# Kernel tuning notes

Hardware: AMD Instinct MI355X
Metric: run time of the kernel (lower is better)

## Reference

```python
import jax, jax.numpy as jnp
import numpy as np

B, D, L, H = 256, 512, 64, 300


def setup_inputs() -> dict:
    key = jax.random.key(0)
    ks = jax.random.split(key, 16)
    s = 0.05  # weight init scale to keep activations sane through ReLU chains
    return {
        "x": jax.random.normal(ks[0], (B, D), jnp.float32),
        "eps": jax.random.normal(ks[1], (B, L), jnp.float32),
        "W": jax.random.normal(ks[2], (D, L), jnp.float32) * s,
        "enc1_w": jax.random.normal(ks[3], (H, D), jnp.float32) * s,
        "enc1_b": jax.random.normal(ks[4], (H,), jnp.float32) * s,
        "enc2_w": jax.random.normal(ks[5], (H, H), jnp.float32) * s,
        "enc2_b": jax.random.normal(ks[6], (H,), jnp.float32) * s,
        "zm_w": jax.random.normal(ks[7], (L, H), jnp.float32) * s,
        "zm_b": jax.random.normal(ks[8], (L,), jnp.float32) * s,
        "zv_w": jax.random.normal(ks[9], (L, H), jnp.float32) * s,
        "zv_b": jax.random.normal(ks[10], (L,), jnp.float32) * s,
        "gen1_w": jax.random.normal(ks[11], (H, L), jnp.float32) * s,
        "gen2_w": jax.random.normal(ks[12], (H, H), jnp.float32) * s,
        "gen2_b": jax.random.normal(ks[13], (H,), jnp.float32) * s,
        "head_w": jax.random.normal(ks[14], (D, H), jnp.float32) * s,
        "head_b": jax.random.normal(ks[15], (D,), jnp.float32) * s,
    }


def reference(x, eps, W, enc1_w, enc1_b, enc2_w, enc2_b, zm_w, zm_b,
              zv_w, zv_b, gen1_w, gen2_w, gen2_b, head_w, head_b):
    # encode: q_z = ReLU(Linear) -> ReLU(Linear)
    h = jax.nn.relu(x @ enc1_w.T + enc1_b)
    h = jax.nn.relu(h @ enc2_w.T + enc2_b)
    z_mean = h @ zm_w.T + zm_b          # [B, L]
    z_log_var = h @ zv_w.T + zv_b       # [B, L]
    # reparameterize (eps passed in for determinism)
    z = z_mean + eps * jnp.exp(0.5 * z_log_var)
    # decode: per-column masked z through shared generator + per-column head,
    # vectorized over the column axis D (mask = W rows)
    masked = z[:, None, :] * W[None, :, :]                       # [B, D, L]
    g1 = jax.nn.relu(jnp.einsum('bdl,hl->bdh', masked, gen1_w))  # [B, D, H]
    g2 = jax.nn.relu(jnp.einsum('bdh,gh->bdg', g1, gen2_w) + gen2_b)
    x_mean = jnp.einsum('bdh,dh->bd', g2, head_w) + head_b       # [B, D]
    return (x_mean, z, z_mean, z_log_var)
```

## Files before the change

kernel.cpp:

```cpp
#include <hip/hip_runtime.h>

typedef unsigned short u16;
typedef unsigned int u32;

typedef __bf16 bf16x8 __attribute__((ext_vector_type(8)));
typedef float f32x4 __attribute__((ext_vector_type(4)));

union V16 { uint4 u; bf16x8 v; u16 s[8]; __bf16 h[8]; };
union F4  { float4 v; float f[4]; };

__device__ __forceinline__ float bf2f(u16 a) {
  union { u32 u; float f; } c; c.u = ((u32)a) << 16; return c.f;
}

#define Z_OFF   131072
#define ZM_OFF  147456
#define ZLV_OFF 163840

#define B1_OFF 0
#define B2_OFF 2560
#define E1_OFF 15360
#define E2_OFF 35840
#define ZMP_OFF 48640
#define ZVP_OFF 51200
#define FRAG_TOTAL 53760
#define WB4  53760
#define XB4  57856
#define H1_4 74240
#define H2_4 84480
#define PACK_THREADS (FRAG_TOTAL + 4096 + 16384)

__device__ __forceinline__ void pack_one(const float* __restrict__ src,
                                         int t, int s, int lane,
                                         int Nsrc, int Ksrc, int rowlen,
                                         uint4* __restrict__ dst) {
  const int n = t * 16 + (lane & 15);
  const int k0 = s * 32 + ((lane >> 4) << 3);
  V16 v;
#pragma unroll
  for (int j = 0; j < 8; ++j) {
    const int k = k0 + j;
    v.h[j] = (n < Nsrc && k < Ksrc) ? (__bf16)src[n * rowlen + k] : (__bf16)0.f;
  }
  *dst = v.u;
}

__device__ __forceinline__ void cvt8(const float* __restrict__ src, uint4* __restrict__ dst) {
  F4 a, b; a.v = *(const float4*)src; b.v = *(const float4*)(src + 4);
  V16 v;
#pragma unroll
  for (int j = 0; j < 4; ++j) { v.h[j] = (__bf16)a.f[j]; v.h[4 + j] = (__bf16)b.f[j]; }
  *dst = v.u;
}

__global__ __launch_bounds__(256) void pack_kernel(
    const float* __restrict__ g1w, const float* __restrict__ g2w,
    const float* __restrict__ e1w, const float* __restrict__ e2w,
    const float* __restrict__ zmw, const float* __restrict__ zvw,
    const float* __restrict__ W,   const float* __restrict__ x,
    uint4* __restrict__ ws4) {
  const int idx = blockIdx.x * 256 + threadIdx.x;
  if (idx >= PACK_THREADS) return;
  const int lane = idx & 63;
  if (idx < B2_OFF) {
    const int f = (idx - B1_OFF) >> 6;
    pack_one(g1w, f >> 1, f & 1, lane, 300, 64, 64, ws4 + idx);
  } else if (idx < E1_OFF) {
    const int f = (idx - B2_OFF) >> 6;
    pack_one(g2w, f / 10, f % 10, lane, 300, 300, 300, ws4 + idx);
  } else if (idx < E2_OFF) {
    const int f = (idx - E1_OFF) >> 6;
    pack_one(e1w, f >> 4, f & 15, lane, 300, 512, 512, ws4 + idx);
  } else if (idx < ZMP_OFF) {
    const int f = (idx - E2_OFF) >> 6;
    pack_one(e2w, f / 10, f % 10, lane, 300, 300, 300, ws4 + idx);
  } else if (idx < ZVP_OFF) {
    const int f = (idx - ZMP_OFF) >> 6;
    pack_one(zmw, f / 10, f % 10, lane, 64, 300, 300, ws4 + idx);
  } else if (idx < FRAG_TOTAL) {
    const int f = (idx - ZVP_OFF) >> 6;
    pack_one(zvw, f / 10, f % 10, lane, 64, 300, 300, ws4 + idx);
  } else if (idx < FRAG_TOTAL + 4096) {
    const int i = idx - FRAG_TOTAL;
    cvt8(W + i * 8, ws4 + WB4 + i);
  } else {
    const int i = idx - FRAG_TOTAL - 4096;
    cvt8(x + i * 8, ws4 + XB4 + i);
  }
}

__global__ __launch_bounds__(256) void enc1_kernel(
    const uint4* __restrict__ xb, const uint4* __restrict__ e1p,
    const float* __restrict__ e1b, u16* __restrict__ h1) {
  __shared__ float red[4 * 320];
  const int wg = blockIdx.x;
  const int rt = wg / 20, nt = wg % 20;
  const int tid = threadIdx.x;
  const int w = tid >> 6, lane = tid & 63, q = lane >> 4, c = lane & 15;
  f32x4 acc = {0.f, 0.f, 0.f, 0.f};
  const int arow = rt * 16 + c;
#pragma unroll
  for (int j = 0; j < 4; ++j) {
    const int s = 4 * w + j;
    V16 a, b;
    a.u = xb[arow * 64 + s * 4 + q];
    b.u = e1p[(nt * 16 + s) * 64 + lane];
    acc = __builtin_amdgcn_mfma_f32_16x16x32_bf16(a.v, b.v, acc, 0, 0, 0);
  }
#pragma unroll
  for (int i = 0; i < 4; ++i) red[w * 320 + lane * 5 + i] = acc[i];
  __syncthreads();
  const int col = nt * 16 + c;
  float t = 0.f;
#pragma unroll
  for (int ww = 0; ww < 4; ++ww) t += red[ww * 320 + lane * 5 + w];
  const float bias = (col < 300) ? e1b[col] : 0.f;
  const int row = rt * 16 + 4 * q + w;
  V16 o; o.h[0] = (col < 300) ? (__bf16)fmaxf(t + bias, 0.f) : (__bf16)0.f;
  h1[row * 320 + col] = o.s[0];
}

__global__ __launch_bounds__(320) void enc2_kernel(
    const uint4* __restrict__ h1, const uint4* __restrict__ e2p,
    const float* __restrict__ e2b, u16* __restrict__ h2) {
  __shared__ float red[5 * 320];
  const int wg = blockIdx.x;
  const int rt = wg / 20, nt = wg % 20;
  const int tid = threadIdx.x;
  const int w = tid >> 6, lane = tid & 63, q = lane >> 4, c = lane & 15;
  f32x4 acc = {0.f, 0.f, 0.f, 0.f};
  const int arow = rt * 16 + c;
#pragma unroll
  for (int j = 0; j < 2; ++j) {
    const int s = 2 * w + j;
    V16 a, b;
    a.u = h1[arow * 40 + s * 4 + q];
    b.u = e2p[(nt * 10 + s) * 64 + lane];
    acc = __builtin_amdgcn_mfma_f32_16x16x32_bf16(a.v, b.v, acc, 0, 0, 0);
  }
#pragma unroll
  for (int i = 0; i < 4; ++i) red[w * 320 + lane * 5 + i] = acc[i];
  __syncthreads();
  if (w < 4) {
    const int col = nt * 16 + c;
    float t = 0.f;
#pragma unroll
    for (int ww = 0; ww < 5; ++ww) t += red[ww * 320 + lane * 5 + w];
    const float bias = (col < 300) ? e2b[col] : 0.f;
    const int row = rt * 16 + 4 * q + w;
    V16 o; o.h[0] = (col < 300) ? (__bf16)fmaxf(t + bias, 0.f) : (__bf16)0.f;
    h2[row * 320 + col] = o.s[0];
  }
}

__global__ __launch_bounds__(320) void ench_kernel(
    const uint4* __restrict__ h2, const float* __restrict__ eps,
    const uint4* __restrict__ zmp, const float* __restrict__ zmb,
    const uint4* __restrict__ zvp, const float* __restrict__ zvb,
    float* __restrict__ out) {
  __shared__ float redm[5 * 320];
  __shared__ float redv[5 * 320];
  const int wg = blockIdx.x;
  const int rt = wg >> 2, t = wg & 3;
  const int tid = threadIdx.x;
  const int w = tid >> 6, lane = tid & 63, q = lane >> 4, c = lane & 15;
  f32x4 am = {0.f, 0.f, 0.f, 0.f}, av = {0.f, 0.f, 0.f, 0.f};
  const int arow = rt * 16 + c;
#pragma unroll
  for (int j = 0; j < 2; ++j) {
    const int s = 2 * w + j;
    V16 a, bm, bv;
    a.u = h2[arow * 40 + s * 4 + q];
    bm.u = zmp[(t * 10 + s) * 64 + lane];
    bv.u = zvp[(t * 10 + s) * 64 + lane];
    am = __builtin_amdgcn_mfma_f32_16x16x32_bf16(a.v, bm.v, am, 0, 0, 0);
    av = __builtin_amdgcn_mfma_f32_16x16x32_bf16(a.v, bv.v, av, 0, 0, 0);
  }
#pragma unroll
  for (int i = 0; i < 4; ++i) {
    redm[w * 320 + lane * 5 + i] = am[i];
    redv[w * 320 + lane * 5 + i] = av[i];
  }
  __syncthreads();
  if (w < 4) {
    const int col = t * 16 + c;
    float tm = 0.f, tv = 0.f;
#pragma unroll
    for (int ww = 0; ww < 5; ++ww) {
      tm += redm[ww * 320 + lane * 5 + w];
      tv += redv[ww * 320 + lane * 5 + w];
    }
    const float zm = tm + zmb[col];
    const float zlv = tv + zvb[col];
    const int gi = (rt * 16 + 4 * q + w) * 64 + col;
    out[ZM_OFF + gi] = zm;
    out[ZLV_OFF + gi] = zlv;
    out[Z_OFF + gi] = zm + eps[gi] * expf(0.5f * zlv);
  }
}

__global__ __launch_bounds__(320, 4) void dec_kernel(
    const float* __restrict__ z,
    const uint4* __restrict__ Wb,
    const uint4* __restrict__ b1p,
    const uint4* __restrict__ b2p,
    const float* __restrict__ g2b,
    const float* __restrict__ hw,
    const float* __restrict__ hb,
    float* __restrict__ xout) {
  __shared__ u16 g1s[32 * 328];
  float* xredf = (float*)g1s;

  const int wg = blockIdx.x;
  const int r0 = wg << 5;
  const int bi = wg >> 4;
  const int d0 = r0 & 511;
  const int tid = threadIdx.x;
  const int u = tid >> 6;
  const int lane = tid & 63;
  const int q = lane >> 4;
  const int c = lane & 15;

  const float* zrow = z + bi * 64;

  bf16x8 bz[4][2];
#pragma unroll
  for (int kf = 0; kf < 2; ++kf) {
    F4 z0, z1;
    z0.v = *(const float4*)(zrow + kf * 32 + q * 8);
    z1.v = *(const float4*)(zrow + kf * 32 + q * 8 + 4);
#pragma unroll
    for (int tt = 0; tt < 4; ++tt) {
      V16 r; r.u = b1p[((4 * u + tt) * 2 + kf) * 64 + lane];
      V16 m;
#pragma unroll
      for (int j = 0; j < 4; ++j) {
        m.h[j]     = (__bf16)(bf2f(r.s[j])     * z0.f[j]);
        m.h[4 + j] = (__bf16)(bf2f(r.s[4 + j]) * z1.f[j]);
      }
      bz[tt][kf] = m.v;
    }
  }
#pragma unroll
  for (int rt = 0; rt < 2; ++rt) {
    const int rowA = rt * 16 + c;
    V16 af0, af1;
    af0.u = Wb[(d0 + rowA) * 8 + q];
    af1.u = Wb[(d0 + rowA) * 8 + 4 + q];
    f32x4 acc[4];
#pragma unroll
    for (int tt = 0; tt < 4; ++tt) acc[tt] = {0.f, 0.f, 0.f, 0.f};
#pragma unroll
    for (int tt = 0; tt < 4; ++tt) {
      acc[tt] = __builtin_amdgcn_mfma_f32_16x16x32_bf16(af0.v, bz[tt][0], acc[tt], 0, 0, 0);
      acc[tt] = __builtin_amdgcn_mfma_f32_16x16x32_bf16(af1.v, bz[tt][1], acc[tt], 0, 0, 0);
    }
    const int rwb = rt * 16 + 4 * q;
#pragma unroll
    for (int tt = 0; tt < 4; ++tt) {
      const int colb = (4 * u + tt) * 16 + c;
#pragma unroll
      for (int i = 0; i < 4; ++i) {
        V16 t; t.h[0] = (__bf16)fmaxf(acc[tt][i], 0.f);
        g1s[(rwb + i) * 328 + colb] = t.s[0];
      }
    }
  }
  __syncthreads();

  f32x4 a3[4][2];
#pragma unroll
  for (int tt = 0; tt < 4; ++tt)
#pragma unroll
    for (int rt = 0; rt < 2; ++rt) a3[tt][rt] = {0.f, 0.f, 0.f, 0.f};
  for (int s = 0; s < 10; ++s) {
    V16 b[4];
#pragma unroll
    for (int tt = 0; tt < 4; ++tt) b[tt].u = b2p[((4 * u + tt) * 10 + s) * 64 + lane];
#pragma unroll
    for (int rt = 0; rt < 2; ++rt) {
      V16 a; a.u = *(const uint4*)&g1s[(rt * 16 + c) * 328 + s * 32 + q * 8];
#pragma unroll
      for (int tt = 0; tt < 4; ++tt)
        a3[tt][rt] = __builtin_amdgcn_mfma_f32_16x16x32_bf16(a.v, b[tt].v, a3[tt][rt], 0, 0, 0);
    }
  }
  float xacc[2][4];
#pragma unroll
  for (int rt = 0; rt < 2; ++rt)
#pragma unroll
    for (int i = 0; i < 4; ++i) xacc[rt][i] = 0.f;
#pragma unroll
  for (int tt = 0; tt < 4; ++tt) {
    const int col = (4 * u + tt) * 16 + c;
    const bool inb = (col < 300);
    const float bias = inb ? g2b[col] : 0.f;
#pragma unroll
    for (int rt = 0; rt < 2; ++rt)
#pragma unroll
      for (int i = 0; i < 4; ++i) {
        const float g2v = fmaxf(a3[tt][rt][i] + bias, 0.f);
        const float h = inb ? hw[(d0 + rt * 16 + 4 * q + i) * 300 + col] : 0.f;
        xacc[rt][i] += g2v * h;
      }
  }
#pragma unroll
  for (int rt = 0; rt < 2; ++rt)
#pragma unroll
    for (int i = 0; i < 4; ++i) {
      float t = xacc[rt][i];
      t += __shfl_xor(t, 1);
      t += __shfl_xor(t, 2);
      t += __shfl_xor(t, 4);
      t += __shfl_xor(t, 8);
      xacc[rt][i] = t;
    }
  __syncthreads();
  if (c < 4) {
#pragma unroll
    for (int rt = 0; rt < 2; ++rt) {
      float t = xacc[rt][0];
      t = (c == 1) ? xacc[rt][1] : t;
      t = (c == 2) ? xacc[rt][2] : t;
      t = (c == 3) ? xacc[rt][3] : t;
      xredf[u * 32 + rt * 16 + 4 * q + c] = t;
    }
  }
  __syncthreads();
  if (tid < 32) {
    float t = hb[d0 + tid];
#pragma unroll
    for (int uu = 0; uu < 5; ++uu) t += xredf[uu * 32 + tid];
    xout[r0 + tid] = t;
  }
}

extern "C" void kernel_launch(void* const* d_in, const int* in_sizes, int n_in,
                              void* d_out, int out_size, void* d_ws, size_t ws_size,
                              hipStream_t stream) {
  const float* x   = (const float*)d_in[0];
  const float* eps = (const float*)d_in[1];
  const float* W   = (const float*)d_in[2];
  const float* e1w = (const float*)d_in[3];
  const float* e1b = (const float*)d_in[4];
  const float* e2w = (const float*)d_in[5];
  const float* e2b = (const float*)d_in[6];
  const float* zmw = (const float*)d_in[7];
  const float* zmb = (const float*)d_in[8];
  const float* zvw = (const float*)d_in[9];
  const float* zvb = (const float*)d_in[10];
  const float* g1w = (const float*)d_in[11];
  const float* g2w = (const float*)d_in[12];
  const float* g2b = (const float*)d_in[13];
  const float* hw  = (const float*)d_in[14];
  const float* hb  = (const float*)d_in[15];
  float* out = (float*)d_out;
  uint4* ws4 = (uint4*)d_ws;

  pack_kernel<<<(PACK_THREADS + 255) / 256, 256, 0, stream>>>(
      g1w, g2w, e1w, e2w, zmw, zvw, W, x, ws4);
  enc1_kernel<<<320, 256, 0, stream>>>(ws4 + XB4, ws4 + E1_OFF, e1b, (u16*)(ws4 + H1_4));
  enc2_kernel<<<320, 320, 0, stream>>>(ws4 + H1_4, ws4 + E2_OFF, e2b, (u16*)(ws4 + H2_4));
  ench_kernel<<<64, 320, 0, stream>>>(ws4 + H2_4, eps,
                                      ws4 + ZMP_OFF, zmb, ws4 + ZVP_OFF, zvb, out);
  dec_kernel<<<4096, 320, 0, stream>>>(out + Z_OFF, ws4 + WB4,
                                       ws4 + B1_OFF, ws4 + B2_OFF,
                                       g2b, hw, hb, out);
}
```

Measured before the change: 162.4 us.

## Fold weight packing into encoder kernels and drop separate pack launch

Removes the standalone pack kernel. Encoder weight fragments are now built on the fly from fp32 with vectorized loads and in-register bf16 conversion, and x is converted into shared memory inside enc1. The decoder-weight packing runs as extra blocks appended to the enc1 launch. This saves one kernel launch and a workspace round trip. In exchange, enc1 blocks do more work and enc2 and ench redo the weight conversion in every block.

```diff
diff --git a/kernel.cpp b/kernel.cpp
--- a/kernel.cpp
+++ b/kernel.cpp
@@ -19,16 +19,11 @@
 
 #define B1_OFF 0
 #define B2_OFF 2560
-#define E1_OFF 15360
-#define E2_OFF 35840
-#define ZMP_OFF 48640
-#define ZVP_OFF 51200
-#define FRAG_TOTAL 53760
-#define WB4  53760
-#define XB4  57856
-#define H1_4 74240
-#define H2_4 84480
-#define PACK_THREADS (FRAG_TOTAL + 4096 + 16384)
+#define WB4   15360
+#define PACK_DEC_TOTAL 19456
+#define PACK_DEC_BLOCKS 76
+#define H1_4 20480
+#define H2_4 30720
 
 __device__ __forceinline__ void pack_one(const float* __restrict__ src,
                                          int t, int s, int lane,
@@ -53,58 +48,73 @@
   *dst = v.u;
 }
 
-__global__ __launch_bounds__(256) void pack_kernel(
+__device__ __forceinline__ uint4 mkfrag(const float* __restrict__ w, int n, int k0,
+                                        int N, int K, int ld) {
+  V16 v;
+  if (n < N && k0 + 7 < K) {
+    F4 a, b;
+    a.v = *(const float4*)(w + n * ld + k0);
+    b.v = *(const float4*)(w + n * ld + k0 + 4);
+#pragma unroll
+    for (int j = 0; j < 4; ++j) { v.h[j] = (__bf16)a.f[j]; v.h[4 + j] = (__bf16)b.f[j]; }
+  } else if (n < N) {
+#pragma unroll
+    for (int j = 0; j < 8; ++j) {
+      const int k = k0 + j;
+      v.h[j] = (k < K) ? (__bf16)w[n * ld + k] : (__bf16)0.f;
+    }
+  } else {
+    v.u = make_uint4(0u, 0u, 0u, 0u);
+  }
+  return v.u;
+}
+
+__global__ __launch_bounds__(256) void enc1_kernel(
+    const float* __restrict__ x,   const float* __restrict__ e1w,
+    const float* __restrict__ e1b, u16* __restrict__ h1,
     const float* __restrict__ g1w, const float* __restrict__ g2w,
-    const float* __restrict__ e1w, const float* __restrict__ e2w,
-    const float* __restrict__ zmw, const float* __restrict__ zvw,
-    const float* __restrict__ W,   const float* __restrict__ x,
-    uint4* __restrict__ ws4) {
-  const int idx = blockIdx.x * 256 + threadIdx.x;
-  if (idx >= PACK_THREADS) return;
-  const int lane = idx & 63;
-  if (idx < B2_OFF) {
-    const int f = (idx - B1_OFF) >> 6;
-    pack_one(g1w, f >> 1, f & 1, lane, 300, 64, 64, ws4 + idx);
-  } else if (idx < E1_OFF) {
-    const int f = (idx - B2_OFF) >> 6;
-    pack_one(g2w, f / 10, f % 10, lane, 300, 300, 300, ws4 + idx);
-  } else if (idx < E2_OFF) {
-    const int f = (idx - E1_OFF) >> 6;
-    pack_one(e1w, f >> 4, f & 15, lane, 300, 512, 512, ws4 + idx);
-  } else if (idx < ZMP_OFF) {
-    const int f = (idx - E2_OFF) >> 6;
-    pack_one(e2w, f / 10, f % 10, lane, 300, 300, 300, ws4 + idx);
-  } else if (idx < ZVP_OFF) {
-    const int f = (idx - ZMP_OFF) >> 6;
-    pack_one(zmw, f / 10, f % 10, lane, 64, 300, 300, ws4 + idx);
-  } else if (idx < FRAG_TOTAL) {
-    const int f = (idx - ZVP_OFF) >> 6;
-    pack_one(zvw, f / 10, f % 10, lane, 64, 300, 300, ws4 + idx);
-  } else if (idx < FRAG_TOTAL + 4096) {
-    const int i = idx - FRAG_TOTAL;
-    cvt8(W + i * 8, ws4 + WB4 + i);
-  } else {
-    const int i = idx - FRAG_TOTAL - 4096;
-    cvt8(x + i * 8, ws4 + XB4 + i);
-  }
-}
-
-__global__ __launch_bounds__(256) void enc1_kernel(
-    const uint4* __restrict__ xb, const uint4* __restrict__ e1p,
-    const float* __restrict__ e1b, u16* __restrict__ h1) {
+    const float* __restrict__ W,   uint4* __restrict__ ws4) {
+  __shared__ uint4 xs[16 * 65];
   __shared__ float red[4 * 320];
-  const int wg = blockIdx.x;
-  const int rt = wg / 20, nt = wg % 20;
+
+  const int blk = blockIdx.x;
   const int tid = threadIdx.x;
+
+  if (blk >= 320) {
+    const int idx = (blk - 320) * 256 + tid;
+    if (idx >= PACK_DEC_TOTAL) return;
+    const int lane = idx & 63;
+    if (idx < B2_OFF) {
+      const int f = idx >> 6;
+      pack_one(g1w, f >> 1, f & 1, lane, 300, 64, 64, ws4 + idx);
+    } else if (idx < WB4) {
+      const int f = (idx - B2_OFF) >> 6;
+      pack_one(g2w, f / 10, f % 10, lane, 300, 300, 300, ws4 + idx);
+    } else {
+      const int i = idx - WB4;
+      cvt8(W + i * 8, ws4 + WB4 + i);
+    }
+    return;
+  }
+
+  const int rt = blk / 20, nt = blk % 20;
   const int w = tid >> 6, lane = tid & 63, q = lane >> 4, c = lane & 15;
+  const int r0 = rt * 16;
+
+  for (int i = tid; i < 1024; i += 256) {
+    const int row = i >> 6, kg = i & 63;
+    cvt8(x + (r0 + row) * 512 + kg * 8, &xs[row * 65 + kg]);
+  }
+  __syncthreads();
+
   f32x4 acc = {0.f, 0.f, 0.f, 0.f};
-  const int arow = rt * 16 + c;
+  const int nbase = nt * 16 + c;
 #pragma unroll
   for (int j = 0; j < 4; ++j) {
     const int s = 4 * w + j;
     V16 a, b;
-    a.u = xb[arow * 64 + s * 4 + q];
-    b.u = e1p[(nt * 16 + s) * 64 + lane];
+    a.u = xs[c * 65 + s * 4 + q];
+    b.u = mkfrag(e1w, nbase, s * 32 + q * 8, 300, 512, 512);
     acc = __builtin_amdgcn_mfma_f32_16x16x32_bf16(a.v, b.v, acc, 0, 0, 0);
   }
 #pragma unroll
@@ -121,7 +131,7 @@
 }
 
 __global__ __launch_bounds__(320) void enc2_kernel(
-    const uint4* __restrict__ h1, const uint4* __restrict__ e2p,
+    const uint4* __restrict__ h1, const float* __restrict__ e2w,
     const float* __restrict__ e2b, u16* __restrict__ h2) {
   __shared__ float red[5 * 320];
   const int wg = blockIdx.x;
@@ -130,12 +140,13 @@
   const int w = tid >> 6, lane = tid & 63, q = lane >> 4, c = lane & 15;
   f32x4 acc = {0.f, 0.f, 0.f, 0.f};
   const int arow = rt * 16 + c;
+  const int nbase = nt * 16 + c;
 #pragma unroll
   for (int j = 0; j < 2; ++j) {
     const int s = 2 * w + j;
     V16 a, b;
     a.u = h1[arow * 40 + s * 4 + q];
-    b.u = e2p[(nt * 10 + s) * 64 + lane];
+    b.u = mkfrag(e2w, nbase, s * 32 + q * 8, 300, 300, 300);
     acc = __builtin_amdgcn_mfma_f32_16x16x32_bf16(a.v, b.v, acc, 0, 0, 0);
   }
 #pragma unroll
@@ -155,8 +166,8 @@
 
 __global__ __launch_bounds__(320) void ench_kernel(
     const uint4* __restrict__ h2, const float* __restrict__ eps,
-    const uint4* __restrict__ zmp, const float* __restrict__ zmb,
-    const uint4* __restrict__ zvp, const float* __restrict__ zvb,
+    const float* __restrict__ zmw, const float* __restrict__ zmb,
+    const float* __restrict__ zvw, const float* __restrict__ zvb,
     float* __restrict__ out) {
   __shared__ float redm[5 * 320];
   __shared__ float redv[5 * 320];
@@ -166,13 +177,14 @@
   const int w = tid >> 6, lane = tid & 63, q = lane >> 4, c = lane & 15;
   f32x4 am = {0.f, 0.f, 0.f, 0.f}, av = {0.f, 0.f, 0.f, 0.f};
   const int arow = rt * 16 + c;
+  const int nbase = t * 16 + c;
 #pragma unroll
   for (int j = 0; j < 2; ++j) {
     const int s = 2 * w + j;
     V16 a, bm, bv;
     a.u = h2[arow * 40 + s * 4 + q];
-    bm.u = zmp[(t * 10 + s) * 64 + lane];
-    bv.u = zvp[(t * 10 + s) * 64 + lane];
+    bm.u = mkfrag(zmw, nbase, s * 32 + q * 8, 64, 300, 300);
+    bv.u = mkfrag(zvw, nbase, s * 32 + q * 8, 64, 300, 300);
     am = __builtin_amdgcn_mfma_f32_16x16x32_bf16(a.v, bm.v, am, 0, 0, 0);
     av = __builtin_amdgcn_mfma_f32_16x16x32_bf16(a.v, bv.v, av, 0, 0, 0);
   }
@@ -357,12 +369,10 @@
   float* out = (float*)d_out;
   uint4* ws4 = (uint4*)d_ws;
 
-  pack_kernel<<<(PACK_THREADS + 255) / 256, 256, 0, stream>>>(
-      g1w, g2w, e1w, e2w, zmw, zvw, W, x, ws4);
-  enc1_kernel<<<320, 256, 0, stream>>>(ws4 + XB4, ws4 + E1_OFF, e1b, (u16*)(ws4 + H1_4));
-  enc2_kernel<<<320, 320, 0, stream>>>(ws4 + H1_4, ws4 + E2_OFF, e2b, (u16*)(ws4 + H2_4));
-  ench_kernel<<<64, 320, 0, stream>>>(ws4 + H2_4, eps,
-                                      ws4 + ZMP_OFF, zmb, ws4 + ZVP_OFF, zvb, out);
+  enc1_kernel<<<320 + PACK_DEC_BLOCKS, 256, 0, stream>>>(
+      x, e1w, e1b, (u16*)(ws4 + H1_4), g1w, g2w, W, ws4);
+  enc2_kernel<<<320, 320, 0, stream>>>(ws4 + H1_4, e2w, e2b, (u16*)(ws4 + H2_4));
+  ench_kernel<<<64, 320, 0, stream>>>(ws4 + H2_4, eps, zmw, zmb, zvw, zvb, out);
   dec_kernel<<<4096, 320, 0, stream>>>(out + Z_OFF, ws4 + WB4,
                                        ws4 + B1_OFF, ws4 + B2_OFF,
                                        g2b, hw, hb, out);
```

Measured after the change: 163.2 us. About the same (+0.5%).
